# Kernel tuning notes

Hardware: AMD Instinct MI355X
Metric: run time of the kernel (lower is better)

## Reference

```python
import jax, jax.numpy as jnp
import numpy as np

N = 50000     # nodes
E = 800000    # edges (before self-loops)
DIN = 128     # input feature dim
DH = 16       # per-head hidden dim (layer 1)
H = 8         # heads (layer 1)
DOUT = 64     # output classes (layer 2, heads=1)


def setup_inputs() -> dict:
    key = jax.random.key(0)
    ks = jax.random.split(key, 10)
    def rn(k, shape, scale=0.1):
        return jax.random.normal(k, shape, dtype=jnp.float32) * scale
    x = jax.random.normal(ks[0], (N, DIN), dtype=jnp.float32)
    edge_index = jax.random.randint(ks[1], (2, E), 0, N, dtype=jnp.int64)
    return {
        "x": x,
        "edge_index": edge_index,
        "W1": rn(ks[2], (DIN, H * DH)),
        "a_src1": rn(ks[3], (H, DH)),
        "a_dst1": rn(ks[4], (H, DH)),
        "b1": jnp.zeros((H * DH,), jnp.float32),
        "W2": rn(ks[5], (H * DH, DOUT)),
        "a_src2": rn(ks[6], (1, DOUT)),
        "a_dst2": rn(ks[7], (1, DOUT)),
        "b2": jnp.zeros((DOUT,), jnp.float32),
    }


def gat_conv(x, src, dst, W, a_src, a_dst, b, heads, out_dim):
    """PyG-style GATConv: edge attention + segment softmax over dst + scatter-add."""
    n = x.shape[0]
    h = (x @ W).reshape(n, heads, out_dim)                 # [N, H, D]
    alpha_src = jnp.sum(h * a_src, axis=-1)                # [N, H]
    alpha_dst = jnp.sum(h * a_dst, axis=-1)                # [N, H]
    e = jax.nn.leaky_relu(alpha_src[src] + alpha_dst[dst], 0.2)  # [Etot, H]
    # numerically-stable segment softmax grouped by destination node
    m = jax.ops.segment_max(e, dst, num_segments=n)        # [N, H]
    ex = jnp.exp(e - m[dst])
    s = jax.ops.segment_sum(ex, dst, num_segments=n)       # [N, H]
    alpha = ex / (s[dst] + 1e-16)                          # [Etot, H]
    msg = h[src] * alpha[..., None]                        # [Etot, H, D]
    out = jax.ops.segment_sum(msg, dst, num_segments=n)    # [N, H, D]
    return out.reshape(n, heads * out_dim) + b


def reference(x, W1, a_src1, a_dst1, b1, W2, a_src2, a_dst2, b2, edge_index):
    # eval mode: F.dropout(p=0.6, training=False) is identity
    loop = jnp.arange(N, dtype=edge_index.dtype)
    src = jnp.concatenate([edge_index[0], loop])  # add_self_loops=True (PyG default)
    dst = jnp.concatenate([edge_index[1], loop])
    h = gat_conv(x, src, dst, W1, a_src1, a_dst1, b1, H, DH)
    h = jax.nn.elu(h)
    h = gat_conv(h, src, dst, W2, a_src2, a_dst2, b2, 1, DOUT)
    return (h, jax.nn.log_softmax(h, axis=1))
```

## Files before the change

kernel.cpp:

```cpp
#include <hip/hip_runtime.h>

#define NN 50000
#define EE 800000
#define ET (EE + NN)
#define NCH ((NN + 255) / 256)

typedef unsigned short ushort_t;
using bf16x8 = __attribute__((ext_vector_type(8))) short;
using f32x4  = __attribute__((ext_vector_type(4))) float;

__device__ __forceinline__ float bf2f(ushort_t u) {
    return __uint_as_float(((unsigned int)u) << 16);
}
__device__ __forceinline__ ushort_t f2bf(float f) {
    unsigned int u = __float_as_uint(f);
    u += 0x7fffu + ((u >> 16) & 1u);
    return (ushort_t)(u >> 16);
}
__device__ __forceinline__ float lrelu(float e) {
    return fmaxf(e, 0.f) + 0.2f * fminf(e, 0.f);
}
__device__ __forceinline__ float ldf(const void* p, int i, bool f32) {
    return f32 ? ((const float*)p)[i] : bf2f(((const ushort_t*)p)[i]);
}

__global__ __launch_bounds__(256) void sniff_kernel(const unsigned int* xw, const int* eiw, int* flags) {
    __shared__ int cnt0, cnt1;
    int t = threadIdx.x;
    if (t == 0) { cnt0 = 0; cnt1 = 0; }
    __syncthreads();
    float v = __uint_as_float(xw[t]);
    float a = fabsf(v);
    if ((a > 1e-6f && a < 1e6f) || v == 0.f) atomicAdd(&cnt0, 1);
    if (eiw[2 * t + 1] != 0) atomicAdd(&cnt1, 1);
    __syncthreads();
    if (t == 0) {
        flags[0] = (cnt0 >= 192) ? 1 : 0;
        flags[1] = (cnt1 <= 16) ? 1 : 0;
    }
}

__device__ __forceinline__ void edge_sd(const int* ei, int i, bool i64, int& s, int& d) {
    if (i < EE) {
        if (i64) { s = ei[2 * i]; d = ei[2 * (EE + i)]; }
        else     { s = ei[i];     d = ei[EE + i]; }
    } else {
        s = d = i - EE;
    }
}

__global__ __launch_bounds__(256) void degree_rank_kernel(const int* ei, int* deg8, int* rank, const int* flags) {
    int i = blockIdx.x * 256 + threadIdx.x;
    if (i >= ET) return;
    bool i64 = flags[1] != 0;
    int g = blockIdx.x & 7;
    int s, d;
    edge_sd(ei, i, i64, s, d);
    rank[i] = atomicAdd(&deg8[(size_t)g * NN + d], 1);
}

__global__ __launch_bounds__(256) void scanA_kernel(const int* __restrict__ deg8, int* __restrict__ chunksum) {
    __shared__ int wsum[4];
    int t = threadIdx.x;
    int node = blockIdx.x * 256 + t;
    int v = 0;
    if (node < NN) {
        #pragma unroll
        for (int g = 0; g < 8; ++g) v += deg8[(size_t)g * NN + node];
    }
    int lane = t & 63, wid = t >> 6;
    #pragma unroll
    for (int off = 1; off < 64; off <<= 1) v += __shfl_xor(v, off);
    if (lane == 0) wsum[wid] = v;
    __syncthreads();
    if (t == 0) chunksum[blockIdx.x] = wsum[0] + wsum[1] + wsum[2] + wsum[3];
}

__global__ __launch_bounds__(256) void scanB_kernel(const int* __restrict__ chunksum, int* __restrict__ chunkoff,
                                                    int* __restrict__ rowptr) {
    __shared__ int wsum[4];
    int t = threadIdx.x;
    int lane = t & 63, wid = t >> 6;
    int v = (t < NCH) ? chunksum[t] : 0;
    int x = v;
    #pragma unroll
    for (int off = 1; off < 64; off <<= 1) {
        int y = __shfl_up(x, off);
        if (lane >= off) x += y;
    }
    if (lane == 63) wsum[wid] = x;
    __syncthreads();
    if (t < 4) {
        int s = wsum[t];
        #pragma unroll
        for (int off = 1; off < 4; off <<= 1) {
            int y = __shfl_up(s, off);
            if (t >= off) s += y;
        }
        wsum[t] = s;
    }
    __syncthreads();
    int incl = x + ((wid > 0) ? wsum[wid - 1] : 0);
    if (t < NCH) chunkoff[t] = incl - v;
    if (t == 255) rowptr[NN] = wsum[3];
}

__global__ __launch_bounds__(256) void scanC_kernel(int* __restrict__ deg8, int* __restrict__ rowptr,
                                                    const int* __restrict__ chunkoff) {
    __shared__ int wsum[4];
    int t = threadIdx.x;
    int node = blockIdx.x * 256 + t;
    int dv[8];
    int v = 0;
    if (node < NN) {
        #pragma unroll
        for (int g = 0; g < 8; ++g) {
            dv[g] = deg8[(size_t)g * NN + node];
            v += dv[g];
        }
    }
    int lane = t & 63, wid = t >> 6;
    int x = v;
    #pragma unroll
    for (int off = 1; off < 64; off <<= 1) {
        int y = __shfl_up(x, off);
        if (lane >= off) x += y;
    }
    if (lane == 63) wsum[wid] = x;
    __syncthreads();
    if (t < 4) {
        int s = wsum[t];
        #pragma unroll
        for (int off = 1; off < 4; off <<= 1) {
            int y = __shfl_up(s, off);
            if (t >= off) s += y;
        }
        wsum[t] = s;
    }
    __syncthreads();
    int excl = x - v + ((wid > 0) ? wsum[wid - 1] : 0);
    if (node < NN) {
        int run = chunkoff[blockIdx.x] + excl;
        rowptr[node] = run;
        #pragma unroll
        for (int g = 0; g < 8; ++g) {
            deg8[(size_t)g * NN + node] = run;
            run += dv[g];
        }
    }
}

__global__ __launch_bounds__(256) void fill_kernel(const int* ei, const int* deg8off, const int* rank,
                                                   int* col, const int* flags) {
    int i = blockIdx.x * 256 + threadIdx.x;
    if (i >= ET) return;
    bool i64 = flags[1] != 0;
    int g = blockIdx.x & 7;
    int s, d;
    edge_sd(ei, i, i64, s, d);
    col[deg8off[(size_t)g * NN + d] + rank[i]] = s;
}

template <bool AEXT, int NCOL, int NH>
__global__ __launch_bounds__(256) void mgemm_kernel(const void* Av, const void* Wv,
                                                    const void* a_src, const void* a_dst,
                                                    ushort_t* outb, float* asrc, float* adst,
                                                    int n, const int* flags) {
    constexpr int K = 128;
    constexpr int NCT = NCOL / 16;
    constexpr int WPAD = 136;
    __shared__ __align__(16) ushort_t Wb[NCOL * WPAD];
    bool f32 = flags[0] != 0;
    int t = threadIdx.x;

    for (int i = t; i < K * NCOL; i += 256) {
        int k = i / NCOL, nc = i % NCOL;
        Wb[nc * WPAD + k] = f32 ? f2bf(((const float*)Wv)[k * NCOL + nc])
                                : ((const ushort_t*)Wv)[k * NCOL + nc];
    }
    __syncthreads();

    int lane = t & 63, wid = t >> 6;
    int m = lane & 15, quad = lane >> 4;
    int rbase = blockIdx.x * 64 + wid * 16;
    int row = rbase + m;
    bool rok = row < n;

    f32x4 acc[NCT];
    #pragma unroll
    for (int c = 0; c < NCT; ++c) acc[c] = (f32x4){0.f, 0.f, 0.f, 0.f};

    #pragma unroll
    for (int kk = 0; kk < K; kk += 32) {
        bf16x8 af;
        if (rok) {
            if (AEXT && !f32) {
                af = *(const bf16x8*)((const ushort_t*)Av + (size_t)row * K + kk + quad * 8);
            } else {
                const float* ap = (const float*)Av + (size_t)row * K + kk + quad * 8;
                #pragma unroll
                for (int j = 0; j < 8; ++j) af[j] = (short)f2bf(ap[j]);
            }
        } else {
            af = (bf16x8){0, 0, 0, 0, 0, 0, 0, 0};
        }
        #pragma unroll
        for (int c = 0; c < NCT; ++c) {
            bf16x8 bf = *(const bf16x8*)(&Wb[(c * 16 + m) * WPAD + kk + quad * 8]);
            acc[c] = __builtin_amdgcn_mfma_f32_16x16x32_bf16(af, bf, acc[c], 0, 0, 0);
        }
    }

    int orow0 = rbase + quad * 4;
    #pragma unroll
    for (int c = 0; c < NCT; ++c) {
        #pragma unroll
        for (int r = 0; r < 4; ++r) {
            int orow = orow0 + r;
            if (orow < n) outb[(size_t)orow * NCOL + c * 16 + m] = f2bf(acc[c][r]);
        }
    }

    if (NH == 8) {
        #pragma unroll
        for (int c = 0; c < NCT; ++c) {
            float as = ldf(a_src, c * 16 + m, f32);
            float ad = ldf(a_dst, c * 16 + m, f32);
            float ps[4], pd[4];
            #pragma unroll
            for (int r = 0; r < 4; ++r) { ps[r] = acc[c][r] * as; pd[r] = acc[c][r] * ad; }
            #pragma unroll
            for (int stp = 1; stp < 16; stp <<= 1) {
                #pragma unroll
                for (int r = 0; r < 4; ++r) {
                    ps[r] += __shfl_xor(ps[r], stp);
                    pd[r] += __shfl_xor(pd[r], stp);
                }
            }
            if (m == 0) {
                #pragma unroll
                for (int r = 0; r < 4; ++r) {
                    int orow = orow0 + r;
                    if (orow < n) {
                        asrc[(size_t)orow * 8 + c] = ps[r];
                        adst[(size_t)orow * 8 + c] = pd[r];
                    }
                }
            }
        }
    } else {
        float ps[4] = {0.f, 0.f, 0.f, 0.f}, pd[4] = {0.f, 0.f, 0.f, 0.f};
        #pragma unroll
        for (int c = 0; c < NCT; ++c) {
            float as = ldf(a_src, c * 16 + m, f32);
            float ad = ldf(a_dst, c * 16 + m, f32);
            #pragma unroll
            for (int r = 0; r < 4; ++r) {
                ps[r] = fmaf(acc[c][r], as, ps[r]);
                pd[r] = fmaf(acc[c][r], ad, pd[r]);
            }
        }
        #pragma unroll
        for (int stp = 1; stp < 16; stp <<= 1) {
            #pragma unroll
            for (int r = 0; r < 4; ++r) {
                ps[r] += __shfl_xor(ps[r], stp);
                pd[r] += __shfl_xor(pd[r], stp);
            }
        }
        if (m == 0) {
            #pragma unroll
            for (int r = 0; r < 4; ++r) {
                int orow = orow0 + r;
                if (orow < n) { asrc[orow] = ps[r]; adst[orow] = pd[r]; }
            }
        }
    }
}

__global__ __launch_bounds__(256) void agg1_kernel(const int* __restrict__ rowptr, const int* __restrict__ col,
                                                   const ushort_t* __restrict__ h1b,
                                                   const float* __restrict__ asrc, const float* __restrict__ adst,
                                                   const void* b1, float* __restrict__ hmid, const int* flags) {
    __shared__ float wle[4][8 * 72];
    __shared__ int loff[4][64];
    bool f32 = flags[0] != 0;
    int lane = threadIdx.x & 63, wid = threadIdx.x >> 6;
    int d = blockIdx.x * 4 + wid;
    if (d >= NN) return;
    int start = rowptr[d], end = rowptr[d + 1];
    int hB = lane >> 3;
    const float4* dp = (const float4*)(adst + (size_t)d * 8);
    float4 ad0 = dp[0], ad1 = dp[1];
    const char* hb = (const char*)h1b + lane * 4;
    float acc0 = 0.f, acc1 = 0.f, ssum = 0.f;
    for (int chunk = start; chunk < end; chunk += 64) {
        int cnt = min(64, end - chunk);
        int c = (chunk + lane < end) ? col[chunk + lane] : 0;
        loff[wid][lane] = c << 8;
        if (lane < cnt) {
            const float4* ap = (const float4*)(asrc + (size_t)c * 8);
            float4 s0 = ap[0], s1 = ap[1];
            wle[wid][0 * 72 + lane] = __expf(lrelu(s0.x + ad0.x));
            wle[wid][1 * 72 + lane] = __expf(lrelu(s0.y + ad0.y));
            wle[wid][2 * 72 + lane] = __expf(lrelu(s0.z + ad0.z));
            wle[wid][3 * 72 + lane] = __expf(lrelu(s0.w + ad0.w));
            wle[wid][4 * 72 + lane] = __expf(lrelu(s1.x + ad1.x));
            wle[wid][5 * 72 + lane] = __expf(lrelu(s1.y + ad1.y));
            wle[wid][6 * 72 + lane] = __expf(lrelu(s1.z + ad1.z));
            wle[wid][7 * 72 + lane] = __expf(lrelu(s1.w + ad1.w));
        }
        #pragma unroll 4
        for (int j = 0; j < cnt; ++j) {
            int off = loff[wid][j];
            float ex = wle[wid][hB * 72 + j];
            unsigned int hv = *(const unsigned int*)(hb + off);
            ssum += ex;
            acc0 = fmaf(ex, __uint_as_float(hv << 16), acc0);
            acc1 = fmaf(ex, __uint_as_float(hv & 0xffff0000u), acc1);
        }
    }
    float inv = 1.f / (ssum + 1e-16f);
    float o0 = fmaf(acc0, inv, ldf(b1, lane * 2, f32));
    float o1 = fmaf(acc1, inv, ldf(b1, lane * 2 + 1, f32));
    o0 = (o0 > 0.f) ? o0 : (__expf(o0) - 1.f);
    o1 = (o1 > 0.f) ? o1 : (__expf(o1) - 1.f);
    *(float2*)(hmid + (size_t)d * 128 + lane * 2) = make_float2(o0, o1);
}

__global__ __launch_bounds__(256) void agg2_kernel(const int* __restrict__ rowptr, const int* __restrict__ col,
                                                   const ushort_t* __restrict__ h2b,
                                                   const float* __restrict__ asrc, const float* __restrict__ adst,
                                                   const void* b2, float* __restrict__ out, const int* flags) {
    __shared__ float wle[4][64];
    __shared__ int loff[4][64];
    bool f32 = flags[0] != 0;
    int lane = threadIdx.x & 63, wid = threadIdx.x >> 6;
    int d = blockIdx.x * 4 + wid;
    if (d >= NN) return;
    int start = rowptr[d], end = rowptr[d + 1];
    float ad = adst[d];
    const char* hb = (const char*)h2b + lane * 2;
    float acc = 0.f, ssum = 0.f;
    for (int chunk = start; chunk < end; chunk += 64) {
        int cnt = min(64, end - chunk);
        int c = (chunk + lane < end) ? col[chunk + lane] : 0;
        loff[wid][lane] = c << 7;
        if (lane < cnt) wle[wid][lane] = __expf(lrelu(asrc[c] + ad));
        #pragma unroll 4
        for (int j = 0; j < cnt; ++j) {
            int off = loff[wid][j];
            float ex = wle[wid][j];
            float hv = bf2f(*(const ushort_t*)(hb + off));
            ssum += ex;
            acc = fmaf(ex, hv, acc);
        }
    }
    float o = acc / (ssum + 1e-16f) + ldf(b2, lane, f32);
    float mm = o;
    #pragma unroll
    for (int off = 1; off < 64; off <<= 1) mm = fmaxf(mm, __shfl_xor(mm, off));
    float texp = __expf(o - mm);
    float ts = texp;
    #pragma unroll
    for (int off = 1; off < 64; off <<= 1) ts += __shfl_xor(ts, off);
    float ls = o - mm - __logf(ts);
    out[(size_t)d * 64 + lane] = o;
    out[(size_t)NN * 64 + (size_t)d * 64 + lane] = ls;
}

extern "C" void kernel_launch(void* const* d_in, const int* in_sizes, int n_in,
                              void* d_out, int out_size, void* d_ws, size_t ws_size,
                              hipStream_t stream) {
    const void* x   = d_in[0];
    const int*  ei  = (const int*)d_in[1];
    const void* W1  = d_in[2];
    const void* as1 = d_in[3];
    const void* ad1 = d_in[4];
    const void* b1  = d_in[5];
    const void* W2  = d_in[6];
    const void* as2 = d_in[7];
    const void* ad2 = d_in[8];
    const void* b2  = d_in[9];
    float* out = (float*)d_out;

    char* w = (char*)d_ws;
    auto alloc = [&](size_t bytes) {
        void* p = (void*)w;
        w += (bytes + 255) & ~(size_t)255;
        return p;
    };
    int* flags    = (int*)alloc(256);
    int* deg8     = (int*)alloc((size_t)8 * NN * 4);
    int* rowptr   = (int*)alloc((size_t)(NN + 1) * 4);
    int* chunksum = (int*)alloc((size_t)NCH * 4);
    int* chunkoff = (int*)alloc((size_t)NCH * 4);
    int* rank     = (int*)alloc((size_t)ET * 4);
    int* colx     = (int*)alloc((size_t)ET * 4);
    ushort_t* h1b = (ushort_t*)alloc((size_t)NN * 128 * 2);
    float* asrc1  = (float*)alloc((size_t)NN * 8 * 4);
    float* adst1  = (float*)alloc((size_t)NN * 8 * 4);
    float* hmid   = (float*)alloc((size_t)NN * 128 * 4);
    ushort_t* h2b = (ushort_t*)alloc((size_t)NN * 64 * 2);
    float* asrc2  = (float*)alloc((size_t)NN * 4);
    float* adst2  = (float*)alloc((size_t)NN * 4);

    sniff_kernel<<<1, 256, 0, stream>>>((const unsigned int*)x, ei, flags);

    hipMemsetAsync(deg8, 0, (size_t)8 * NN * 4, stream);
    degree_rank_kernel<<<(ET + 255) / 256, 256, 0, stream>>>(ei, deg8, rank, flags);
    scanA_kernel<<<NCH, 256, 0, stream>>>(deg8, chunksum);
    scanB_kernel<<<1, 256, 0, stream>>>(chunksum, chunkoff, rowptr);
    scanC_kernel<<<NCH, 256, 0, stream>>>(deg8, rowptr, chunkoff);
    fill_kernel<<<(ET + 255) / 256, 256, 0, stream>>>(ei, deg8, rank, colx, flags);

    int gblocks = (NN + 63) / 64;
    mgemm_kernel<true, 128, 8><<<gblocks, 256, 0, stream>>>(x, W1, as1, ad1, h1b, asrc1, adst1, NN, flags);
    agg1_kernel<<<(NN + 3) / 4, 256, 0, stream>>>(rowptr, colx, h1b, asrc1, adst1, b1, hmid, flags);

    mgemm_kernel<false, 64, 1><<<gblocks, 256, 0, stream>>>((const void*)hmid, W2, as2, ad2, h2b, asrc2, adst2, NN, flags);
    agg2_kernel<<<(NN + 3) / 4, 256, 0, stream>>>(rowptr, colx, h2b, asrc2, adst2, b2, out, flags);
}
```

Measured before the change: 271.5 us.

## Pretranspose weights once, read B from global, store hidden layer as bf16

A new small kernel converts and transposes W1/W2 to bf16 once, so each GEMM block no longer fills a shared-memory copy of the weights or waits on a barrier. The GEMM now preloads all A fragments with vectorized loads and reads B fragments straight from global memory, where they are expected to stay in cache. The intermediate activation hmid is written as bf16 instead of fp32, which halves the traffic between agg1 and the second GEMM. The trade-offs are an extra kernel launch, more global or L2 loads per block for the weights, and the intermediate rounded to bf16, which the old code already did when loading it into the GEMM.

```diff
diff --git a/kernel.cpp b/kernel.cpp
--- a/kernel.cpp
+++ b/kernel.cpp
@@ -161,53 +161,76 @@
     col[deg8off[(size_t)g * NN + d] + rank[i]] = s;
 }
 
+__global__ __launch_bounds__(256) void wtprep_kernel(const void* W1v, const void* W2v,
+                                                     ushort_t* Wt1, ushort_t* Wt2, const int* flags) {
+    bool f32 = flags[0] != 0;
+    int i = blockIdx.x * 256 + threadIdx.x;
+    if (i < 128 * 128) {
+        int k = i >> 7, nc = i & 127;
+        ushort_t v = f32 ? f2bf(((const float*)W1v)[i]) : ((const ushort_t*)W1v)[i];
+        Wt1[nc * 128 + k] = v;
+    }
+    int j = i - 128 * 128;
+    if (j >= 0 && j < 128 * 64) {
+        int k = j >> 6, nc = j & 63;
+        ushort_t v = f32 ? f2bf(((const float*)W2v)[j]) : ((const ushort_t*)W2v)[j];
+        Wt2[nc * 128 + k] = v;
+    }
+}
+
 template <bool AEXT, int NCOL, int NH>
-__global__ __launch_bounds__(256) void mgemm_kernel(const void* Av, const void* Wv,
+__global__ __launch_bounds__(256) void mgemm_kernel(const void* Av, const ushort_t* __restrict__ Wt,
                                                     const void* a_src, const void* a_dst,
                                                     ushort_t* outb, float* asrc, float* adst,
                                                     int n, const int* flags) {
     constexpr int K = 128;
     constexpr int NCT = NCOL / 16;
-    constexpr int WPAD = 136;
-    __shared__ __align__(16) ushort_t Wb[NCOL * WPAD];
     bool f32 = flags[0] != 0;
+    bool af32 = AEXT && f32;
     int t = threadIdx.x;
-
-    for (int i = t; i < K * NCOL; i += 256) {
-        int k = i / NCOL, nc = i % NCOL;
-        Wb[nc * WPAD + k] = f32 ? f2bf(((const float*)Wv)[k * NCOL + nc])
-                                : ((const ushort_t*)Wv)[k * NCOL + nc];
-    }
-    __syncthreads();
-
     int lane = t & 63, wid = t >> 6;
     int m = lane & 15, quad = lane >> 4;
     int rbase = blockIdx.x * 64 + wid * 16;
     int row = rbase + m;
     bool rok = row < n;
 
+    bf16x8 af[4];
+    if (rok) {
+        if (!af32) {
+            const ushort_t* ap = (const ushort_t*)Av + (size_t)row * K + quad * 8;
+            #pragma unroll
+            for (int kk = 0; kk < 4; ++kk) af[kk] = *(const bf16x8*)(ap + kk * 32);
+        } else {
+            const float* ap = (const float*)Av + (size_t)row * K + quad * 8;
+            #pragma unroll
+            for (int kk = 0; kk < 4; ++kk) {
+                float4 q0 = *(const float4*)(ap + kk * 32);
+                float4 q1 = *(const float4*)(ap + kk * 32 + 4);
+                bf16x8 v;
+                v[0] = (short)f2bf(q0.x); v[1] = (short)f2bf(q0.y);
+                v[2] = (short)f2bf(q0.z); v[3] = (short)f2bf(q0.w);
+                v[4] = (short)f2bf(q1.x); v[5] = (short)f2bf(q1.y);
+                v[6] = (short)f2bf(q1.z); v[7] = (short)f2bf(q1.w);
+                af[kk] = v;
+            }
+        }
+    } else {
+        #pragma unroll
+        for (int kk = 0; kk < 4; ++kk) af[kk] = (bf16x8){0, 0, 0, 0, 0, 0, 0, 0};
+    }
+
     f32x4 acc[NCT];
     #pragma unroll
     for (int c = 0; c < NCT; ++c) acc[c] = (f32x4){0.f, 0.f, 0.f, 0.f};
 
-    #pragma unroll
-    for (int kk = 0; kk < K; kk += 32) {
-        bf16x8 af;
-        if (rok) {
-            if (AEXT && !f32) {
-                af = *(const bf16x8*)((const ushort_t*)Av + (size_t)row * K + kk + quad * 8);
-            } else {
-                const float* ap = (const float*)Av + (size_t)row * K + kk + quad * 8;
-                #pragma unroll
-                for (int j = 0; j < 8; ++j) af[j] = (short)f2bf(ap[j]);
-            }
-        } else {
-            af = (bf16x8){0, 0, 0, 0, 0, 0, 0, 0};
-        }
-        #pragma unroll
-        for (int c = 0; c < NCT; ++c) {
-            bf16x8 bf = *(const bf16x8*)(&Wb[(c * 16 + m) * WPAD + kk + quad * 8]);
-            acc[c] = __builtin_amdgcn_mfma_f32_16x16x32_bf16(af, bf, acc[c], 0, 0, 0);
+    const ushort_t* wp = Wt + (size_t)m * K + quad * 8;
+    #pragma unroll
+    for (int c = 0; c < NCT; ++c) {
+        const ushort_t* wc = wp + (size_t)c * 16 * K;
+        #pragma unroll
+        for (int kk = 0; kk < 4; ++kk) {
+            bf16x8 bf = *(const bf16x8*)(wc + kk * 32);
+            acc[c] = __builtin_amdgcn_mfma_f32_16x16x32_bf16(af[kk], bf, acc[c], 0, 0, 0);
         }
     }
 
@@ -281,7 +304,7 @@
 __global__ __launch_bounds__(256) void agg1_kernel(const int* __restrict__ rowptr, const int* __restrict__ col,
                                                    const ushort_t* __restrict__ h1b,
                                                    const float* __restrict__ asrc, const float* __restrict__ adst,
-                                                   const void* b1, float* __restrict__ hmid, const int* flags) {
+                                                   const void* b1, ushort_t* __restrict__ hmidb, const int* flags) {
     __shared__ float wle[4][8 * 72];
     __shared__ int loff[4][64];
     bool f32 = flags[0] != 0;
@@ -325,7 +348,8 @@
     float o1 = fmaf(acc1, inv, ldf(b1, lane * 2 + 1, f32));
     o0 = (o0 > 0.f) ? o0 : (__expf(o0) - 1.f);
     o1 = (o1 > 0.f) ? o1 : (__expf(o1) - 1.f);
-    *(float2*)(hmid + (size_t)d * 128 + lane * 2) = make_float2(o0, o1);
+    unsigned int pk = ((unsigned int)f2bf(o1) << 16) | (unsigned int)f2bf(o0);
+    *(unsigned int*)(hmidb + (size_t)d * 128 + lane * 2) = pk;
 }
 
 __global__ __launch_bounds__(256) void agg2_kernel(const int* __restrict__ rowptr, const int* __restrict__ col,
@@ -397,10 +421,12 @@
     int* chunkoff = (int*)alloc((size_t)NCH * 4);
     int* rank     = (int*)alloc((size_t)ET * 4);
     int* colx     = (int*)alloc((size_t)ET * 4);
+    ushort_t* Wt1 = (ushort_t*)alloc((size_t)128 * 128 * 2);
+    ushort_t* Wt2 = (ushort_t*)alloc((size_t)64 * 128 * 2);
     ushort_t* h1b = (ushort_t*)alloc((size_t)NN * 128 * 2);
     float* asrc1  = (float*)alloc((size_t)NN * 8 * 4);
     float* adst1  = (float*)alloc((size_t)NN * 8 * 4);
-    float* hmid   = (float*)alloc((size_t)NN * 128 * 4);
+    ushort_t* hmidb = (ushort_t*)alloc((size_t)NN * 128 * 2);
     ushort_t* h2b = (ushort_t*)alloc((size_t)NN * 64 * 2);
     float* asrc2  = (float*)alloc((size_t)NN * 4);
     float* adst2  = (float*)alloc((size_t)NN * 4);
@@ -413,11 +439,12 @@
     scanB_kernel<<<1, 256, 0, stream>>>(chunksum, chunkoff, rowptr);
     scanC_kernel<<<NCH, 256, 0, stream>>>(deg8, rowptr, chunkoff);
     fill_kernel<<<(ET + 255) / 256, 256, 0, stream>>>(ei, deg8, rank, colx, flags);
+    wtprep_kernel<<<(128 * 128 + 128 * 64 + 255) / 256, 256, 0, stream>>>(W1, W2, Wt1, Wt2, flags);
 
     int gblocks = (NN + 63) / 64;
-    mgemm_kernel<true, 128, 8><<<gblocks, 256, 0, stream>>>(x, W1, as1, ad1, h1b, asrc1, adst1, NN, flags);
-    agg1_kernel<<<(NN + 3) / 4, 256, 0, stream>>>(rowptr, colx, h1b, asrc1, adst1, b1, hmid, flags);
-
-    mgemm_kernel<false, 64, 1><<<gblocks, 256, 0, stream>>>((const void*)hmid, W2, as2, ad2, h2b, asrc2, adst2, NN, flags);
+    mgemm_kernel<true, 128, 8><<<gblocks, 256, 0, stream>>>(x, Wt1, as1, ad1, h1b, asrc1, adst1, NN, flags);
+    agg1_kernel<<<(NN + 3) / 4, 256, 0, stream>>>(rowptr, colx, h1b, asrc1, adst1, b1, hmidb, flags);
+
+    mgemm_kernel<false, 64, 1><<<gblocks, 256, 0, stream>>>((const void*)hmidb, Wt2, as2, ad2, h2b, asrc2, adst2, NN, flags);
     agg2_kernel<<<(NN + 3) / 4, 256, 0, stream>>>(rowptr, colx, h2b, asrc2, adst2, b2, out, flags);
 }
```

Result: faster. 265.1 us (-2.3%).
